# Kernel optimization log

Hardware: AMD Instinct MI355X
Metric: run time of the kernel (lower is better)

## Reference

```python
import jax, jax.numpy as jnp
import numpy as np

B, N, DIM_IN, DIM_K, DIM_V, NH = 2, 2048, 1024, 1024, 1024, 16

def setup_inputs() -> dict:
    key = jax.random.key(0)
    ks = jax.random.split(key, 7)
    s_in = 1.0 / np.sqrt(DIM_IN)
    return {
        "x": jax.random.normal(ks[0], (B, N, DIM_IN), dtype=jnp.float32),
        "Wq": jax.random.uniform(ks[1], (DIM_IN, DIM_K), jnp.float32, -s_in, s_in),
        "bq": jax.random.uniform(ks[2], (DIM_K,), jnp.float32, -s_in, s_in),
        "Wk": jax.random.uniform(ks[3], (DIM_IN, DIM_K), jnp.float32, -s_in, s_in),
        "bk": jax.random.uniform(ks[4], (DIM_K,), jnp.float32, -s_in, s_in),
        "Wv": jax.random.uniform(ks[5], (DIM_IN, DIM_V), jnp.float32, -s_in, s_in),
        "bv": jax.random.uniform(ks[6], (DIM_V,), jnp.float32, -s_in, s_in),
    }

def reference(x, Wq, bq, Wk, bk, Wv, bv):
    b, n, _ = x.shape
    dk = DIM_K // NH
    dv = DIM_V // NH
    scale = 1.0 / np.sqrt(dk)
    # project and split heads: [b, nh, n, dk]
    q = (x @ Wq + bq).reshape(b, n, NH, dk).transpose(0, 2, 1, 3)
    k = (x @ Wk + bk).reshape(b, n, NH, dk).transpose(0, 2, 1, 3)
    v = (x @ Wv + bv).reshape(b, n, NH, dv).transpose(0, 2, 1, 3)
    dist = jnp.einsum('bhqd,bhkd->bhqk', q, k) * scale  # [b,nh,n,n]
    dist = jax.nn.softmax(dist, axis=-1)
    att = jnp.einsum('bhqk,bhkd->bhqd', dist, v)
    return att.transpose(0, 2, 1, 3).reshape(b, n, DIM_V)
```

## Files before the change

### kernel.cpp

```cpp
#include <hip/hip_runtime.h>

#define DI __device__ __forceinline__

typedef unsigned short u16;
typedef short short8 __attribute__((ext_vector_type(8)));
typedef float f32x2 __attribute__((ext_vector_type(2)));
typedef float f32x4 __attribute__((ext_vector_type(4)));
typedef float f32x16 __attribute__((ext_vector_type(16)));
typedef u16 u16x4 __attribute__((ext_vector_type(4)));
typedef unsigned u32x4 __attribute__((ext_vector_type(4)));
typedef int i32x2 __attribute__((ext_vector_type(2)));

DI u16 f2bf(float f){
    unsigned u = __builtin_bit_cast(unsigned, f);
    u += 0x7FFFu + ((u >> 16) & 1u);
    return (u16)(u >> 16);
}
DI float bf2f(u16 b){
    unsigned u = ((unsigned)b) << 16;
    return __builtin_bit_cast(float, u);
}

#if defined(__has_builtin)
#if __has_builtin(__builtin_amdgcn_global_load_lds)
#define HAS_GLL 1
#endif
#if __has_builtin(__builtin_amdgcn_exp2f)
#define HAS_EXP2 1
#endif
#if __has_builtin(__builtin_amdgcn_permlane32_swap)
#define HAS_PL32 1
#endif
#endif

DI void async16(u16* lds, const u16* g){
#ifdef HAS_GLL
    __builtin_amdgcn_global_load_lds(
        (const __attribute__((address_space(1))) unsigned int*)g,
        (__attribute__((address_space(3))) unsigned int*)lds, 16, 0, 0);
#else
    *(short8*)lds = *(const short8*)g;
#endif
}

DI float ex2(float x){
#ifdef HAS_EXP2
    return __builtin_amdgcn_exp2f(x);
#else
    return exp2f(x);
#endif
}

DI unsigned cvtpk(float lo, float hi){
    unsigned r;
    asm("v_cvt_pk_bf16_f32 %0, %1, %2" : "=v"(r) : "v"(lo), "v"(hi));
    return r;
}

DI i32x2 plswap(int a, int b){
#ifdef HAS_PL32
    return __builtin_amdgcn_permlane32_swap(a, b, false, false);
#else
    i32x2 r;
    int ax = __shfl_xor(a, 32), bx = __shfl_xor(b, 32);
    int hi = (threadIdx.x & 63) >> 5;
    r[0] = hi ? bx : a;
    r[1] = hi ? b : ax;
    return r;
#endif
}

#define SEQ   2048
#define DIN   1024
#define MTOT  4096
#define QSCALE 0.18033688011112042f

__global__ void k_prep(const float* __restrict__ x,
                       const float* __restrict__ Wq, const float* __restrict__ Wk,
                       const float* __restrict__ Wv,
                       u16* __restrict__ xb, u16* __restrict__ Wt3){
    __shared__ float t[32][33];
    int bid = blockIdx.x, tid = threadIdx.x;
    if (bid < 4096){
        int i = (bid * 256 + tid) * 4;
        f32x4 v = *(const f32x4*)(x + i);
        u16x4 o;
        #pragma unroll
        for (int j = 0; j < 4; j++) o[j] = f2bf(v[j]);
        *(u16x4*)(xb + i) = o;
    } else {
        int tb = bid - 4096;
        int z  = tb >> 10;
        int t2 = tb & 1023;
        const float* W = (z == 0) ? Wq : (z == 1) ? Wk : Wv;
        u16* Wt = Wt3 + (size_t)z * DIN * DIN;
        int tx = tid & 31, ty = tid >> 5;
        int n0 = (t2 & 31) * 32, k0 = (t2 >> 5) * 32;
        #pragma unroll
        for (int i = 0; i < 4; i++)
            t[ty + i*8][tx] = W[(size_t)(k0 + ty + i*8) * DIN + n0 + tx];
        __syncthreads();
        #pragma unroll
        for (int i = 0; i < 4; i++)
            Wt[(size_t)(n0 + ty + i*8) * DIN + k0 + tx] = f2bf(t[tx][ty + i*8]);
    }
}

__global__ __launch_bounds__(256, 3) void k_projf(const u16* __restrict__ A,
                                                  const u16* __restrict__ Wt3,
                                                  const float* __restrict__ bq,
                                                  const float* __restrict__ bk,
                                                  const float* __restrict__ bv,
                                                  u16* __restrict__ qb,
                                                  u16* __restrict__ kb,
                                                  u16* __restrict__ vtb){
    __shared__ __align__(16) u16 As[2][4096];
    __shared__ __align__(16) u16 Bs[2][4096];
    int tid = threadIdx.x;
    int l = tid & 63, w = tid >> 6;
    int lq = l & 15, lg = l >> 4;
    int wm = w >> 1, wn = w & 1;

    int bid = blockIdx.y * 32 + blockIdx.x;
    int g = bid & 7, i = bid >> 3;
    int mx = g * 4 + (i & 3);
    int by = i >> 2;

    int mat = by >> 3;
    int m0 = mx * 128, n0 = (by & 7) * 128;
    const u16* Bt = Wt3 + (size_t)mat * DIN * DIN;
    const float* bias = (mat == 0) ? bq : (mat == 1) ? bk : bv;

    int r0 = tid >> 2, c0 = (tid & 3) * 8;
    const u16* ap0 = A  + (size_t)(m0 + r0)      * DIN + c0;
    const u16* ap1 = A  + (size_t)(m0 + 64 + r0) * DIN + c0;
    const u16* bp0 = Bt + (size_t)(n0 + r0)      * DIN + c0;
    const u16* bp1 = Bt + (size_t)(n0 + 64 + r0) * DIN + c0;
    int d0 = tid * 8, d1 = 2048 + tid * 8;

#define PSTAGE(bi) {                                              \
    async16(&As[bi][d0], ap0); async16(&As[bi][d1], ap1);         \
    async16(&Bs[bi][d0], bp0); async16(&Bs[bi][d1], bp1);         \
    ap0 += 32; ap1 += 32; bp0 += 32; bp1 += 32; }

    f32x4 acc[4][4] = {};
    PSTAGE(0)

    for (int t = 0; t < 32; t++){
        int cur = t & 1;
        if (t + 1 < 32) PSTAGE(cur ^ 1)
        if (t == 0){
            asm volatile("s_waitcnt vmcnt(4)" ::: "memory");
            __builtin_amdgcn_s_barrier();
        }

        short8 af[4], bf[4];
        #pragma unroll
        for (int f = 0; f < 4; f++){
            af[f] = *(const short8*)&As[cur][(wm*64 + f*16 + lq) * 32 + lg * 8];
            bf[f] = *(const short8*)&Bs[cur][(wn*64 + f*16 + lq) * 32 + lg * 8];
        }
        __builtin_amdgcn_s_setprio(1);
        #pragma unroll
        for (int fm = 0; fm < 4; fm++)
            #pragma unroll
            for (int fn = 0; fn < 4; fn++)
                acc[fm][fn] = __builtin_amdgcn_mfma_f32_16x16x32_bf16(af[fm], bf[fn], acc[fm][fn], 0, 0, 0);
        __builtin_amdgcn_s_setprio(0);

        asm volatile("s_waitcnt vmcnt(0)" ::: "memory");
        __builtin_amdgcn_s_barrier();
    }
#undef PSTAGE

    if (mat == 2){
        for (int fn = 0; fn < 4; fn++){
            int cc = n0 + wn*64 + fn*16 + lq;
            float bvv = bias[cc];
            int hh = cc >> 6, d = cc & 63;
            for (int fm = 0; fm < 4; fm++){
                int mbase = m0 + wm*64 + fm*16 + lg*4;
                int b = mbase >> 11, n = mbase & 2047;
                u16x4 pv;
                for (int r = 0; r < 4; r++) pv[r] = f2bf(acc[fm][fn][r] + bvv);
                *(u16x4*)&vtb[((size_t)(b*16 + hh) * 64 + d) * SEQ + n] = pv;
            }
        }
    } else {
        u16* dst = (mat == 0) ? qb : kb;
        float sc = (mat == 0) ? QSCALE : 1.0f;
        u16* Cs = &As[0][0];
        float bvv[4];
        #pragma unroll
        for (int fn = 0; fn < 4; fn++) bvv[fn] = bias[n0 + wn*64 + fn*16 + lq];

        for (int fm = 0; fm < 4; fm++){
            __syncthreads();
            #pragma unroll
            for (int fn = 0; fn < 4; fn++){
                int c = wn*64 + fn*16 + lq;
                #pragma unroll
                for (int r = 0; r < 4; r++)
                    Cs[(wm*16 + lg*4 + r)*136 + c] = f2bf((acc[fm][fn][r] + bvv[fn]) * sc);
            }
            __syncthreads();
            #pragma unroll
            for (int j = 0; j < 2; j++){
                int wr = (tid >> 4) + j*16;
                int coloff = (tid & 15) * 8;
                int ng = m0 + (wr >> 4)*64 + fm*16 + (wr & 15);
                int b = ng >> 11, n = ng & 2047;
                int cg = n0 + coloff;
                int hh = cg >> 6, d = cg & 63;
                *(short8*)&dst[((size_t)(b*16 + hh) * SEQ + n) * 64 + d] =
                    *(const short8*)&Cs[wr*136 + coloff];
            }
        }
    }
}

#define MFMA32(a, b, c) __builtin_amdgcn_mfma_f32_32x32x16_bf16(a, b, c, 0, 0, 0)

#define MAKE_PA(dst, S, base) {                                   \
    unsigned a0 = cvtpk(S[base+0], S[base+1]);                    \
    unsigned a1 = cvtpk(S[base+2], S[base+3]);                    \
    unsigned b0 = cvtpk(S[base+4], S[base+5]);                    \
    unsigned b1 = cvtpk(S[base+6], S[base+7]);                    \
    i32x2 r0 = plswap((int)a0, (int)b0);                          \
    i32x2 r1 = plswap((int)a1, (int)b1);                          \
    u32x4 wv = {(unsigned)r0[0], (unsigned)r1[0],                 \
                (unsigned)r0[1], (unsigned)r1[1]};                \
    dst = __builtin_bit_cast(short8, wv); }

template<int SPLIT>
__global__ __launch_bounds__(256, 4) void k_attn(const u16* __restrict__ Q,
                                                 const u16* __restrict__ K,
                                                 const u16* __restrict__ Vt,
                                                 float* __restrict__ out,
                                                 u16* __restrict__ po,
                                                 float* __restrict__ mls){
    __shared__ __align__(16) u16 Ks[2][4096];
    __shared__ __align__(16) u16 Vs[3][4096];

    int tid = threadIdx.x, l = tid & 63, w = tid >> 6;
    int lq = l & 31, hi = l >> 5;

    int bid = (blockIdx.z * 32 + blockIdx.y) * 16 + blockIdx.x;
    const int nwg = 512 * SPLIT;
    int d = (bid & 7) * (nwg >> 3) + (bid >> 3);
    const int perbh = 16 * SPLIT;
    int bh = d / perbh;
    int rem = d - bh * perbh;
    int sp = rem >> 4;
    int qx = rem & 15;

    int b = bh >> 4, h = bh & 15;
    int q0 = qx * 128 + w * 32;
    int kvb = sp * (SEQ / SPLIT);
    const int NT = (SEQ / SPLIT) / 64;

    const u16* Qb = Q  + (size_t)bh * SEQ * 64;
    const u16* Kb = K  + (size_t)bh * SEQ * 64;
    const u16* Vb = Vt + (size_t)bh * 64 * SEQ;

    int row0 = tid >> 3;
    int c0   = (tid & 7) ^ (row0 & 7);
    const u16* kp0 = Kb + (size_t)(kvb + row0)      * 64 + c0 * 8;
    const u16* kp1 = Kb + (size_t)(kvb + row0 + 32) * 64 + c0 * 8;
    const u16* vp0 = Vb + (size_t)row0        * SEQ + kvb + c0 * 8;
    const u16* vp1 = Vb + (size_t)(row0 + 32) * SEQ + kvb + c0 * 8;
    int d0 = tid * 8, d1 = 2048 + tid * 8;

#define STAGEK(bi) {                                              \
    async16(&Ks[bi][d0], kp0); async16(&Ks[bi][d1], kp1);         \
    kp0 += 64*64; kp1 += 64*64; }
#define STAGEV(bi) {                                              \
    async16(&Vs[bi][d0], vp0); async16(&Vs[bi][d1], vp1);         \
    vp0 += 64; vp1 += 64; }

    short8 qf[4];
    #pragma unroll
    for (int ks = 0; ks < 4; ks++)
        qf[ks] = *(const short8*)(Qb + (size_t)(q0 + lq) * 64 + ks*16 + hi*8);

    STAGEK(0) STAGEV(0)

    float m = 0.f;
    float ls = 0.f;
    f32x16 o0 = {}, o1 = {};
    short8 pa0, pa1, pa2, pa3;
    int rx = (lq & 7) << 4;

    for (int t = 0; t < NT; t++){
        int kc = t & 1;
        if (t + 1 < NT){ STAGEK(kc ^ 1) STAGEV((t + 1) % 3) }
        if (t == 0){
            if (NT > 1) asm volatile("s_waitcnt vmcnt(4)" ::: "memory");
            else        asm volatile("s_waitcnt vmcnt(0)" ::: "memory");
            __builtin_amdgcn_s_barrier();
        }

        if (t > 0){
            const char* vB = (const char*)&Vs[(t + 2) % 3][0];
            __builtin_amdgcn_s_setprio(1);
            #pragma unroll
            for (int kct = 0; kct < 4; kct++){
                short8 pf = (kct == 0) ? pa0 : (kct == 1) ? pa1 : (kct == 2) ? pa2 : pa3;
                int cb = ((kct*2 + hi) << 4) ^ rx;
                short8 v0 = *(const short8*)(vB + lq*128      + cb);
                short8 v1 = *(const short8*)(vB + (32+lq)*128 + cb);
                o0 = MFMA32(pf, v0, o0);
                o1 = MFMA32(pf, v1, o1);
            }
            __builtin_amdgcn_s_setprio(0);
        }

        const char* kB = (const char*)&Ks[kc][0];
        f32x16 st0 = {}, st1 = {};
        __builtin_amdgcn_s_setprio(1);
        #pragma unroll
        for (int ks = 0; ks < 4; ks++){
            int cb = ((ks*2 + hi) << 4) ^ rx;
            short8 ka = *(const short8*)(kB + lq*128        + cb);
            short8 kb = *(const short8*)(kB + (32+lq)*128   + cb);
            st0 = MFMA32(ka, qf[ks], st0);
            st1 = MFMA32(kb, qf[ks], st1);
        }
        __builtin_amdgcn_s_setprio(0);

        if (m != 0.f){
            #pragma unroll
            for (int r = 0; r < 16; r++){ st0[r] -= m; st1[r] -= m; }
        }

        f32x2 ps = {0.f, 0.f};
        #pragma unroll
        for (int r = 0; r < 16; r += 2){
            st0[r]   = ex2(st0[r]);
            st0[r+1] = ex2(st0[r+1]);
            st1[r]   = ex2(st1[r]);
            st1[r+1] = ex2(st1[r+1]);
            f32x2 a = {st0[r], st0[r+1]};
            f32x2 c = {st1[r], st1[r+1]};
            ps += a + c;
        }
        float psum = ps[0] + ps[1];
        psum += __shfl_xor(psum, 32);

        if (__any(ls + psum > 1.0e30f)){
            const float dn = 5.421010862427522e-20f;
            ls *= dn; psum *= dn;
            #pragma unroll
            for (int r = 0; r < 16; r++){
                o0[r] *= dn; o1[r] *= dn;
                st0[r] *= dn; st1[r] *= dn;
            }
            m += 64.f;
        }
        ls += psum;

        MAKE_PA(pa0, st0, 0)
        MAKE_PA(pa1, st0, 8)
        MAKE_PA(pa2, st1, 0)
        MAKE_PA(pa3, st1, 8)

        asm volatile("s_waitcnt vmcnt(0)" ::: "memory");
        __builtin_amdgcn_s_barrier();
    }

    {
        const char* vB = (const char*)&Vs[(NT + 2) % 3][0];
        __builtin_amdgcn_s_setprio(1);
        #pragma unroll
        for (int kct = 0; kct < 4; kct++){
            short8 pf = (kct == 0) ? pa0 : (kct == 1) ? pa1 : (kct == 2) ? pa2 : pa3;
            int cb = ((kct*2 + hi) << 4) ^ rx;
            short8 v0 = *(const short8*)(vB + lq*128      + cb);
            short8 v1 = *(const short8*)(vB + (32+lq)*128 + cb);
            o0 = MFMA32(pf, v0, o0);
            o1 = MFMA32(pf, v1, o1);
        }
        __builtin_amdgcn_s_setprio(0);
    }

    if (SPLIT == 1){
        #pragma unroll
        for (int r = 0; r < 16; r++){
            int row = (r & 3) + 8*(r >> 2) + 4*hi;
            float inv = 1.0f / __shfl(ls, row);
            float* op = out + ((size_t)b * SEQ + (q0 + row)) * 1024 + h*64 + lq;
            op[0]  = o0[r] * inv;
            op[32] = o1[r] * inv;
        }
    } else {
        u16* pb = po + (size_t)sp * MTOT * 1024;
        #pragma unroll
        for (int r = 0; r < 16; r++){
            int row = (r & 3) + 8*(r >> 2) + 4*hi;
            u16* op = pb + ((size_t)b * SEQ + (q0 + row)) * 1024 + h*64 + lq;
            op[0]  = f2bf(o0[r]);
            op[32] = f2bf(o1[r]);
        }
        if (hi == 0){
            float* mp = mls + (((size_t)sp*32 + bh) * SEQ + (q0 + lq)) * 2;
            mp[0] = m; mp[1] = ls;
        }
    }
#undef STAGEK
#undef STAGEV
}

template<int S>
__global__ __launch_bounds__(256) void k_comb(const u16* __restrict__ po,
                                              const float* __restrict__ mls,
                                              float* __restrict__ out){
    size_t i = ((size_t)blockIdx.x * 256 + threadIdx.x) * 4;
    size_t row = i >> 10;
    int col = (int)(i & 1023);
    int b = (int)(row >> 11), n = (int)(row & 2047);
    int bh = b*16 + (col >> 6);

    float mv[S], lv[S], wv[S];
    float M = -INFINITY;
    #pragma unroll
    for (int s = 0; s < S; s++){
        const float* p = mls + (((size_t)s*32 + bh) * SEQ + n) * 2;
        mv[s] = p[0]; lv[s] = p[1];
        M = fmaxf(M, mv[s]);
    }
    float L = 0.f;
    #pragma unroll
    for (int s = 0; s < S; s++){ wv[s] = ex2(mv[s] - M); L += wv[s] * lv[s]; }
    float inv = 1.0f / L;
    f32x4 acc = {};
    #pragma unroll
    for (int s = 0; s < S; s++){
        u16x4 v = *(const u16x4*)(po + (size_t)s * MTOT * 1024 + i);
        #pragma unroll
        for (int j = 0; j < 4; j++) acc[j] += wv[s] * bf2f(v[j]);
    }
    acc *= inv;
    *(f32x4*)(out + i) = acc;
}

extern "C" void kernel_launch(void* const* d_in, const int* in_sizes, int n_in,
                              void* d_out, int out_size, void* d_ws, size_t ws_size,
                              hipStream_t stream){
    const float* x  = (const float*)d_in[0];
    const float* Wq = (const float*)d_in[1];
    const float* bq = (const float*)d_in[2];
    const float* Wk = (const float*)d_in[3];
    const float* bk = (const float*)d_in[4];
    const float* Wv = (const float*)d_in[5];
    const float* bv = (const float*)d_in[6];
    float* out = (float*)d_out;

    const size_t MB = (size_t)1 << 20;
    if (ws_size < 38 * MB) return;

    char* ws = (char*)d_ws;
    u16* xb   = (u16*)(ws);
    u16* wt3  = (u16*)(ws +  8 * MB);
    u16* qb   = (u16*)(ws + 14 * MB);
    u16* kb   = (u16*)(ws + 22 * MB);
    u16* vtb  = (u16*)(ws + 30 * MB);
    int S = (ws_size >= 38 * MB + 2 * 9 * MB) ? 2 : 1;
    u16* po    = (u16*)(ws + 38 * MB);
    float* mls = (float*)(ws + 38 * MB + (size_t)S * 8 * MB);

    k_prep<<<7168, 256, 0, stream>>>(x, Wq, Wk, Wv, xb, wt3);

    k_projf<<<dim3(32, 24), 256, 0, stream>>>(xb, wt3, bq, bk, bv, qb, kb, vtb);

    if (S == 2){
        k_attn<2><<<dim3(16, 32, 2), 256, 0, stream>>>(qb, kb, vtb, out, po, mls);
        k_comb<2><<<4096, 256, 0, stream>>>(po, mls, out);
    } else {
        k_attn<1><<<dim3(16, 32, 1), 256, 0, stream>>>(qb, kb, vtb, out, po, mls);
    }
}
```

Before: 94.82 us.

## Compute softmax row sums with MFMA against ones and check overflow every four tiles

The softmax denominator is now accumulated on the matrix cores by multiplying the bf16 probability fragments by a ones vector, instead of summing the exponentials with VALU adds and a cross-lane shuffle every tile. The overflow rescale check reads the MFMA-accumulated sums only every fourth tile, which removes per-tile reductions and a wave vote. The cost is one extra MFMA per PV step. The sum is also taken over bf16-rounded probabilities, so it matches the numerator's rounding rather than the fp32 sum. Delaying the overflow check could let values grow larger between checks before rescaling.

```diff
diff --git a/kernel.cpp b/kernel.cpp
--- a/kernel.cpp
+++ b/kernel.cpp
@@ -283,11 +283,14 @@
     for (int ks = 0; ks < 4; ks++)
         qf[ks] = *(const short8*)(Qb + (size_t)(q0 + lq) * 64 + ks*16 + hi*8);
 
+    short8 onesf;
+    #pragma unroll
+    for (int j = 0; j < 8; j++) onesf[j] = (short)0x3F80;
+
     STAGEK(0) STAGEV(0)
 
     float m = 0.f;
-    float ls = 0.f;
-    f32x16 o0 = {}, o1 = {};
+    f32x16 o0 = {}, o1 = {}, lsa = {};
     short8 pa0, pa1, pa2, pa3;
     int rx = (lq & 7) << 4;
 
@@ -309,8 +312,9 @@
                 int cb = ((kct*2 + hi) << 4) ^ rx;
                 short8 v0 = *(const short8*)(vB + lq*128      + cb);
                 short8 v1 = *(const short8*)(vB + (32+lq)*128 + cb);
-                o0 = MFMA32(pf, v0, o0);
-                o1 = MFMA32(pf, v1, o1);
+                o0  = MFMA32(pf, v0, o0);
+                o1  = MFMA32(pf, v1, o1);
+                lsa = MFMA32(pf, onesf, lsa);
             }
             __builtin_amdgcn_s_setprio(0);
         }
@@ -333,36 +337,37 @@
             for (int r = 0; r < 16; r++){ st0[r] -= m; st1[r] -= m; }
         }
 
-        f32x2 ps = {0.f, 0.f};
-        #pragma unroll
-        for (int r = 0; r < 16; r += 2){
-            st0[r]   = ex2(st0[r]);
-            st0[r+1] = ex2(st0[r+1]);
-            st1[r]   = ex2(st1[r]);
-            st1[r+1] = ex2(st1[r+1]);
-            f32x2 a = {st0[r], st0[r+1]};
-            f32x2 c = {st1[r], st1[r+1]};
-            ps += a + c;
-        }
-        float psum = ps[0] + ps[1];
-        psum += __shfl_xor(psum, 32);
-
-        if (__any(ls + psum > 1.0e30f)){
-            const float dn = 5.421010862427522e-20f;
-            ls *= dn; psum *= dn;
-            #pragma unroll
-            for (int r = 0; r < 16; r++){
-                o0[r] *= dn; o1[r] *= dn;
-                st0[r] *= dn; st1[r] *= dn;
-            }
-            m += 64.f;
-        }
-        ls += psum;
+        #pragma unroll
+        for (int r = 0; r < 16; r++){
+            st0[r] = ex2(st0[r]);
+            st1[r] = ex2(st1[r]);
+        }
 
         MAKE_PA(pa0, st0, 0)
         MAKE_PA(pa1, st0, 8)
         MAKE_PA(pa2, st1, 0)
         MAKE_PA(pa3, st1, 8)
+
+        if ((t & 3) == 3){
+            float mx0 = fmaxf(fmaxf(lsa[0], lsa[5]), fmaxf(lsa[10], lsa[15]));
+            float mx1 = fmaxf(fmaxf(lsa[1], lsa[4]), fmaxf(lsa[11], lsa[14]));
+            float mx2 = fmaxf(fmaxf(lsa[2], lsa[7]), fmaxf(lsa[8],  lsa[13]));
+            float mx3 = fmaxf(fmaxf(lsa[3], lsa[6]), fmaxf(lsa[9],  lsa[12]));
+            if (__any(fmaxf(fmaxf(mx0, mx1), fmaxf(mx2, mx3)) > 1.0e30f)){
+                const float dn = 5.421010862427522e-20f;
+                #pragma unroll
+                for (int r = 0; r < 16; r++){
+                    o0[r] *= dn; o1[r] *= dn; lsa[r] *= dn;
+                }
+                #pragma unroll
+                for (int r = 0; r < 16; r++){ st0[r] *= dn; st1[r] *= dn; }
+                MAKE_PA(pa0, st0, 0)
+                MAKE_PA(pa1, st0, 8)
+                MAKE_PA(pa2, st1, 0)
+                MAKE_PA(pa3, st1, 8)
+                m += 64.f;
+            }
+        }
 
         asm volatile("s_waitcnt vmcnt(0)" ::: "memory");
         __builtin_amdgcn_s_barrier();
@@ -377,8 +382,9 @@
             int cb = ((kct*2 + hi) << 4) ^ rx;
             short8 v0 = *(const short8*)(vB + lq*128      + cb);
             short8 v1 = *(const short8*)(vB + (32+lq)*128 + cb);
-            o0 = MFMA32(pf, v0, o0);
-            o1 = MFMA32(pf, v1, o1);
+            o0  = MFMA32(pf, v0, o0);
+            o1  = MFMA32(pf, v1, o1);
+            lsa = MFMA32(pf, onesf, lsa);
         }
         __builtin_amdgcn_s_setprio(0);
     }
@@ -387,7 +393,7 @@
         #pragma unroll
         for (int r = 0; r < 16; r++){
             int row = (r & 3) + 8*(r >> 2) + 4*hi;
-            float inv = 1.0f / __shfl(ls, row);
+            float inv = 1.0f / lsa[r];
             float* op = out + ((size_t)b * SEQ + (q0 + row)) * 1024 + h*64 + lq;
             op[0]  = o0[r] * inv;
             op[32] = o1[r] * inv;
@@ -401,9 +407,13 @@
             op[0]  = f2bf(o0[r]);
             op[32] = f2bf(o1[r]);
         }
-        if (hi == 0){
-            float* mp = mls + (((size_t)sp*32 + bh) * SEQ + (q0 + lq)) * 2;
-            mp[0] = m; mp[1] = ls;
+        if (lq == 0){
+            #pragma unroll
+            for (int r = 0; r < 16; r++){
+                int row = (r & 3) + 8*(r >> 2) + 4*hi;
+                float* mp = mls + (((size_t)sp*32 + bh) * SEQ + (q0 + row)) * 2;
+                mp[0] = m; mp[1] = lsa[r];
+            }
         }
     }
 #undef STAGEK
```

Result: slower. 97.42 us (+2.7%).
